# Kernel tuning notes

Measured on AMD Instinct MI355X. Metric: run time of the kernel, lower is better.

## Reference

```python
import jax, jax.numpy as jnp
import numpy as np

N = 262144   # collocation points (512x512 grid equivalent)
H = 64       # MLP hidden width
PI = np.float32(np.pi)


def setup_inputs() -> dict:
    key = jax.random.key(0)
    ks = jax.random.split(key, 6)
    def glorot(k, shp):
        scale = np.float32(np.sqrt(2.0 / (shp[0] + shp[1])))
        return jax.random.normal(k, shp, jnp.float32) * scale
    return {
        "points": jax.random.uniform(ks[0], (N, 2), jnp.float32),  # (x, t) in [0,1]^2
        "W1": glorot(ks[1], (2, H)), "b1": jnp.zeros((H,), jnp.float32),
        "W2": glorot(ks[2], (H, H)), "b2": jnp.zeros((H,), jnp.float32),
        "W3": glorot(ks[3], (H, H)), "b3": jnp.zeros((H,), jnp.float32),
        "Wo": glorot(ks[4], (H, 1)), "bo": jnp.zeros((1,), jnp.float32),
    }


def _mlp(pt, W1, b1, W2, b2, W3, b3, Wo, bo):
    # pt: [2] -> scalar u(x, t)
    h = jnp.tanh(pt @ W1 + b1)
    h = jnp.tanh(h @ W2 + b2)
    h = jnp.tanh(h @ W3 + b3)
    return (h @ Wo + bo)[0]


def reference(points, W1, b1, W2, b2, W3, b3, Wo, bo):
    params = (W1, b1, W2, b2, W3, b3, Wo, bo)
    dt = points.dtype
    keep_t = jnp.array([0.0, 1.0], dt)   # points * [0,1]
    set_x1 = jnp.array([1.0, 0.0], dt)   # + [1,0] -> (1, t)

    def psi_fn(pt):
        x, t = pt[0], pt[1]
        pt1t = pt * keep_t + set_x1                    # boundary point (1, t)
        u = _mlp(pt, *params)                          # u(x, t)
        u_1t = _mlp(pt1t, *params)                     # u(1, t)
        u1t_x = jax.grad(lambda p: _mlp(p, *params))(pt1t)[0]  # du/dx at (1, t)
        return (2.0 * x * jnp.sin(PI * t)
                + (t * t - t) * (x * x - x) * (u - u_1t - u1t_x))

    def loss_point(pt):
        x, t = pt[0], pt[1]
        psi, g1 = jax.value_and_grad(psi_fn)(pt)       # g1 = (psi_x, psi_t)
        # TF's tape.gradient sums over components of dpsi_dxdt, so:
        # h = grad(psi_x + psi_t) = (psi_xx + psi_tx, psi_xt + psi_tt)
        h = jax.grad(lambda p: jnp.sum(jax.grad(psi_fn)(p)))(pt)
        s = jnp.sin(PI * t)
        res = (h[0] + h[1] + psi * g1[0]
               - s * (2.0 - PI * PI * x * x + 2.0 * x ** 3 * s))
        return jnp.abs(res)

    return jnp.mean(jax.vmap(loss_point)(points))
```

## Files before the change

### kernel.cpp

```cpp
#include <hip/hip_runtime.h>
#include <math.h>

typedef _Float16 half_t;
typedef half_t half8 __attribute__((ext_vector_type(8)));
typedef __fp16 fp16x2 __attribute__((ext_vector_type(2)));
typedef float f32x4 __attribute__((ext_vector_type(4)));
typedef float f32x2 __attribute__((ext_vector_type(2)));

#define PI_F 3.14159265358979323846f

__device__ __forceinline__ f32x2 splat2(float s) { return f32x2{s, s}; }
__device__ __forceinline__ f32x2 fma2(f32x2 a, f32x2 b, f32x2 c) {
    return __builtin_elementwise_fma(a, b, c);
}

__device__ __forceinline__ f32x2 ftanh2(f32x2 z) {
    const f32x2 m = z * splat2(2.8853900817779268f);
    f32x2 t;
    t[0] = exp2f(m[0]);
    t[1] = exp2f(m[1]);
    const f32x2 s = t + splat2(1.f);
    f32x2 r;
    r[0] = __builtin_amdgcn_rcpf(s[0]);
    r[1] = __builtin_amdgcn_rcpf(s[1]);
    return fma2(splat2(-2.f), r, splat2(1.f));
}

__global__ __launch_bounds__(256) void pinn_main(
    const float* __restrict__ pts,
    const float* __restrict__ W1, const float* __restrict__ b1,
    const float* __restrict__ b2, const float* __restrict__ b3,
    const half_t* __restrict__ wsH,
    float* __restrict__ partial)
{
    __shared__ __align__(16) half_t J[192 * 64];
    __shared__ float ubuf[9][16];

    const int tid = threadIdx.x;
    const int l   = tid & 63;
    const int w   = tid >> 6;
    const int q   = l >> 4;
    const int i   = l & 15;
    const int ja  = w * 16 + i;
    const int jb  = w * 16 + q * 4;

    const int rb0 = i * 64 + ((q ^ (i & 7)) << 3);
    const int rb1 = i * 64 + (((4 + q) ^ (i & 7)) << 3);
    const int wbase = i * 64 + ((((w * 2 + (q >> 1)) ^ (i & 7))) << 3) + (q & 1) * 4;

    const half8 w2a = *(const half8*)(wsH + ja * 64 + q * 8);
    const half8 w2b = *(const half8*)(wsH + ja * 64 + 32 + q * 8);
    const half8 w3a = *(const half8*)(wsH + 4096 + ja * 64 + q * 8);
    const half8 w3b = *(const half8*)(wsH + 4096 + ja * 64 + 32 + q * 8);

    const float4 w04 = *(const float4*)(W1 + jb);
    const float4 w14 = *(const float4*)(W1 + 64 + jb);
    const float4 b14 = *(const float4*)(b1 + jb);
    const float4 b24 = *(const float4*)(b2 + jb);
    const float4 b34 = *(const float4*)(b3 + jb);

    half8 wo0 = {0, 0, 0, 0, 0, 0, 0, 0};
    half8 wo1 = {0, 0, 0, 0, 0, 0, 0, 0};
    if (i == 0) {
        wo0 = *(const half8*)(wsH + 8192 + q * 8);
        wo1 = *(const half8*)(wsH + 8192 + 32 + q * 8);
    }

    auto stc = [&](int c, f32x2 v01, f32x2 v23) {
        uint2 d;
        d.x = __builtin_bit_cast(unsigned int,
                                 __builtin_amdgcn_cvt_pkrtz(v01[0], v01[1]));
        d.y = __builtin_bit_cast(unsigned int,
                                 __builtin_amdgcn_cvt_pkrtz(v23[0], v23[1]));
        *(uint2*)(&J[wbase + c * 1024]) = d;
    };

    const f32x2 w0a = {w04.x, w04.y}, w0b = {w04.z, w04.w};
    const f32x2 w1a = {w14.x, w14.y}, w1b = {w14.z, w14.w};
    const f32x2 bba = {b14.x, b14.y}, bbb = {b14.z, b14.w};

    float bsum = 0.f;

    #pragma unroll 1
    for (int pass = 0; pass < 2; ++pass) {
        const int pbase = blockIdx.x * 32 + pass * 16;

        const float2 xy = *(const float2*)(pts + 2 * (pbase + i));
        const float X = xy.x, T = xy.y;

        {
            const f32x2 zva = fma2(splat2(X), w0a, fma2(splat2(T), w1a, bba));
            const f32x2 zvb = fma2(splat2(X), w0b, fma2(splat2(T), w1b, bbb));
            const f32x2 aa = ftanh2(zva), ab = ftanh2(zvb);
            const f32x2 d1a = splat2(1.f) - aa * aa, d1b = splat2(1.f) - ab * ab;
            const f32x2 d2a = splat2(-2.f) * aa * d1a, d2b = splat2(-2.f) * ab * d1b;
            stc(0, aa, ab);
            stc(1, d1a * w0a, d1b * w0b);
            stc(2, d1a * w1a, d1b * w1b);
            stc(3, d2a * w0a * w0a, d2b * w0b * w0b);
            stc(4, d2a * w0a * w1a, d2b * w0b * w1b);
            stc(5, d2a * w1a * w1a, d2b * w1b * w1b);
        }
        {
            const f32x2 zva = fma2(splat2(T), w1a, bba + w0a);
            const f32x2 zvb = fma2(splat2(T), w1b, bbb + w0b);
            const f32x2 aa = ftanh2(zva), ab = ftanh2(zvb);
            const f32x2 e1a = splat2(1.f) - aa * aa, e1b = splat2(1.f) - ab * ab;
            const f32x2 e2a = splat2(-2.f) * aa * e1a, e2b = splat2(-2.f) * ab * e1b;
            const f32x2 e3a = splat2(-2.f) * (e1a * e1a + aa * e2a);
            const f32x2 e3b = splat2(-2.f) * (e1b * e1b + ab * e2b);
            stc(6, aa, ab);
            stc(7, e1a * w0a, e1b * w0b);
            stc(8, e1a * w1a, e1b * w1b);
            stc(9, e2a * w0a * w1a, e2b * w0b * w1b);
            stc(10, e2a * w1a * w1a, e2b * w1b * w1b);
            stc(11, e3a * w0a * w1a * w1a, e3b * w0b * w1b * w1b);
        }

        auto layer_step = [&](const half8 A0, const half8 A1, const float4 b4,
                              bool combine) {
            __syncthreads();
            const f32x4 zb = {b4.x, b4.y, b4.z, b4.w};
            const f32x4 z0 = {0.f, 0.f, 0.f, 0.f};
            f32x4 acc[12];
            #pragma unroll
            for (int c = 0; c < 12; ++c) {
                const half8 f0 = *(const half8*)(&J[rb0 + c * 1024]);
                const half8 f1 = *(const half8*)(&J[rb1 + c * 1024]);
                f32x4 z = (c == 0 || c == 6) ? zb : z0;
                z = __builtin_amdgcn_mfma_f32_16x16x32_f16(A0, f0, z, 0, 0, 0);
                z = __builtin_amdgcn_mfma_f32_16x16x32_f16(A1, f1, z, 0, 0, 0);
                acc[c] = z;
            }
            __syncthreads();

            {
                const f32x2 zva = {acc[0][0], acc[0][1]}, zvb = {acc[0][2], acc[0][3]};
                const f32x2 aa = ftanh2(zva), ab = ftanh2(zvb);
                const f32x2 d1a = splat2(1.f) - aa * aa, d1b = splat2(1.f) - ab * ab;
                const f32x2 d2a = splat2(-2.f) * aa * d1a, d2b = splat2(-2.f) * ab * d1b;
                const f32x2 zxa = {acc[1][0], acc[1][1]}, zxb = {acc[1][2], acc[1][3]};
                const f32x2 zta = {acc[2][0], acc[2][1]}, ztb = {acc[2][2], acc[2][3]};
                const f32x2 zxxa = {acc[3][0], acc[3][1]}, zxxb = {acc[3][2], acc[3][3]};
                const f32x2 zxta = {acc[4][0], acc[4][1]}, zxtb = {acc[4][2], acc[4][3]};
                const f32x2 ztta = {acc[5][0], acc[5][1]}, zttb = {acc[5][2], acc[5][3]};
                stc(0, aa, ab);
                stc(1, d1a * zxa, d1b * zxb);
                stc(2, d1a * zta, d1b * ztb);
                stc(3, fma2(d2a * zxa, zxa, d1a * zxxa), fma2(d2b * zxb, zxb, d1b * zxxb));
                stc(4, fma2(d2a * zxa, zta, d1a * zxta), fma2(d2b * zxb, ztb, d1b * zxtb));
                stc(5, fma2(d2a * zta, zta, d1a * ztta), fma2(d2b * ztb, ztb, d1b * zttb));
            }
            {
                const f32x2 zva = {acc[6][0], acc[6][1]}, zvb = {acc[6][2], acc[6][3]};
                const f32x2 aa = ftanh2(zva), ab = ftanh2(zvb);
                const f32x2 e1a = splat2(1.f) - aa * aa, e1b = splat2(1.f) - ab * ab;
                const f32x2 e2a = splat2(-2.f) * aa * e1a, e2b = splat2(-2.f) * ab * e1b;
                const f32x2 e3a = splat2(-2.f) * (e1a * e1a + aa * e2a);
                const f32x2 e3b = splat2(-2.f) * (e1b * e1b + ab * e2b);
                const f32x2 zxa  = {acc[7][0], acc[7][1]},  zxb  = {acc[7][2], acc[7][3]};
                const f32x2 zta  = {acc[8][0], acc[8][1]},  ztb  = {acc[8][2], acc[8][3]};
                const f32x2 zxta = {acc[9][0], acc[9][1]},  zxtb = {acc[9][2], acc[9][3]};
                const f32x2 ztta = {acc[10][0], acc[10][1]}, zttb = {acc[10][2], acc[10][3]};
                const f32x2 zxtta = {acc[11][0], acc[11][1]}, zxttb = {acc[11][2], acc[11][3]};
                if (combine) {
                    stc(6, aa + e1a * zxa, ab + e1b * zxb);
                    stc(7, fma2(e2a * zxa, zta, fma2(e1a, zxta, e1a * zta)),
                           fma2(e2b * zxb, ztb, fma2(e1b, zxtb, e1b * ztb)));
                    stc(8, fma2(e2a * zta, zta,
                                fma2(e1a, ztta,
                                     fma2(e3a * zxa, zta * zta,
                                          fma2(e2a, fma2(splat2(2.f) * zxta, zta,
                                                         zxa * ztta),
                                               e1a * zxtta)))),
                           fma2(e2b * ztb, ztb,
                                fma2(e1b, zttb,
                                     fma2(e3b * zxb, ztb * ztb,
                                          fma2(e2b, fma2(splat2(2.f) * zxtb, ztb,
                                                         zxb * zttb),
                                               e1b * zxttb)))));
                } else {
                    stc(6, aa, ab);
                    stc(7, e1a * zxa, e1b * zxb);
                    stc(8, e1a * zta, e1b * ztb);
                    stc(9, fma2(e2a * zxa, zta, e1a * zxta),
                           fma2(e2b * zxb, ztb, e1b * zxtb));
                    stc(10, fma2(e2a * zta, zta, e1a * ztta),
                            fma2(e2b * ztb, ztb, e1b * zttb));
                    stc(11,
                        fma2(e3a * zxa, zta * zta,
                             fma2(e2a, fma2(splat2(2.f) * zxta, zta, zxa * ztta),
                                  e1a * zxtta)),
                        fma2(e3b * zxb, ztb * ztb,
                             fma2(e2b, fma2(splat2(2.f) * zxtb, ztb, zxb * zttb),
                                  e1b * zxttb)));
                }
            }
        };
        layer_step(w2a, w2b, b24, false);
        layer_step(w3a, w3b, b34, true);
        __syncthreads();

        if (w < 3) {
            #pragma unroll
            for (int k3 = 0; k3 < 3; ++k3) {
                const int c = w * 3 + k3;
                const half8 f0 = *(const half8*)(&J[rb0 + c * 1024]);
                const half8 f1 = *(const half8*)(&J[rb1 + c * 1024]);
                f32x4 z = {0.f, 0.f, 0.f, 0.f};
                z = __builtin_amdgcn_mfma_f32_16x16x32_f16(wo0, f0, z, 0, 0, 0);
                z = __builtin_amdgcn_mfma_f32_16x16x32_f16(wo1, f1, z, 0, 0, 0);
                if (q == 0) ubuf[c][i] = z[0];
            }
        }
        __syncthreads();

        if (tid < 16) {
            const float x = X, t = T;
            float U[9];
            #pragma unroll
            for (int c = 0; c < 9; ++c) U[c] = ubuf[c][tid];

            const float D   = U[0] - U[6];
            const float Dx  = U[1];
            const float Dt  = U[2] - U[7];
            const float Dxx = U[3];
            const float Dxt = U[4];
            const float Dtt = U[5] - U[8];

            const float s  = __builtin_amdgcn_sinf(0.5f * t);
            const float cc = __builtin_amdgcn_cosf(0.5f * t);
            const float A  = t * t - t,  Ap = 2.f * t - 1.f;
            const float B  = x * x - x,  Bp = 2.f * x - 1.f;

            const float psi    = 2.f * x * s + A * B * D;
            const float psi_x  = 2.f * s + A * (Bp * D + B * Dx);
            const float psi_xx = A * (2.f * D + 2.f * Bp * Dx + B * Dxx);
            const float psi_xt = 2.f * PI_F * cc + Ap * (Bp * D + B * Dx)
                               + A * (Bp * Dt + B * Dxt);
            const float psi_tt = -2.f * PI_F * PI_F * x * s + 2.f * B * D
                               + 2.f * Ap * B * Dt + A * B * Dtt;

            const float forcing = s * (2.f - PI_F * PI_F * x * x
                                       + 2.f * x * x * x * s);
            float s4 = fabsf(psi_xx + 2.f * psi_xt + psi_tt + psi * psi_x - forcing);
            s4 += __shfl_xor(s4, 1, 64);
            s4 += __shfl_xor(s4, 2, 64);
            s4 += __shfl_xor(s4, 4, 64);
            s4 += __shfl_xor(s4, 8, 64);
            if (tid == 0) bsum += s4;
        }
    }

    if (tid == 0) partial[blockIdx.x] = bsum;
}

__global__ __launch_bounds__(256) void pinn_prep(
    const float* __restrict__ W2, const float* __restrict__ W3,
    const float* __restrict__ Wo, half_t* __restrict__ wsH)
{
    const int tid = threadIdx.x;
    for (int idx = tid; idx < 4096; idx += 256) {
        const int n = idx >> 6, k = idx & 63;
        wsH[idx]        = (half_t)W2[k * 64 + n];
        wsH[4096 + idx] = (half_t)W3[k * 64 + n];
    }
    if (tid < 64) wsH[8192 + tid] = (half_t)Wo[tid];
}

__global__ __launch_bounds__(256) void pinn_reduce(
    const float* __restrict__ partial, float* __restrict__ out,
    int nblocks, float invN)
{
    __shared__ float sd[256];
    float s = 0.f;
    for (int i = threadIdx.x; i < nblocks; i += 256) s += partial[i];
    sd[threadIdx.x] = s;
    __syncthreads();
    #pragma unroll
    for (int off = 128; off > 0; off >>= 1) {
        if (threadIdx.x < off) sd[threadIdx.x] += sd[threadIdx.x + off];
        __syncthreads();
    }
    if (threadIdx.x == 0) out[0] = sd[0] * invN;
}

extern "C" void kernel_launch(void* const* d_in, const int* in_sizes, int n_in,
                              void* d_out, int out_size, void* d_ws, size_t ws_size,
                              hipStream_t stream)
{
    const float* pts = (const float*)d_in[0];
    const float* W1  = (const float*)d_in[1];
    const float* b1  = (const float*)d_in[2];
    const float* W2  = (const float*)d_in[3];
    const float* b2  = (const float*)d_in[4];
    const float* W3  = (const float*)d_in[5];
    const float* b3  = (const float*)d_in[6];
    const float* Wo  = (const float*)d_in[7];

    const int nPts    = in_sizes[0] / 2;
    const int nBlocks = nPts / 32;

    half_t* wsH     = (half_t*)d_ws;
    float*  partial = (float*)((char*)d_ws + 32768);

    pinn_prep<<<1, 256, 0, stream>>>(W2, W3, Wo, wsH);
    pinn_main<<<nBlocks, 256, 0, stream>>>(pts, W1, b1, b2, b3, wsH, partial);
    pinn_reduce<<<1, 256, 0, stream>>>(partial, (float*)d_out, nBlocks,
                                       1.f / (float)nPts);
}
```

Measured before the change: 129.4 us.

## Propagate directional derivative along (1,1) instead of separate x/t second derivatives

```diff
diff --git a/kernel.cpp b/kernel.cpp
--- a/kernel.cpp
+++ b/kernel.cpp
@@ -33,8 +33,8 @@
     const half_t* __restrict__ wsH,
     float* __restrict__ partial)
 {
-    __shared__ __align__(16) half_t J[192 * 64];
-    __shared__ float ubuf[9][16];
+    __shared__ __align__(16) half_t J[160 * 64];
+    __shared__ float ubuf[7][16];
 
     const int tid = threadIdx.x;
     const int l   = tid & 63;
@@ -89,6 +89,7 @@
         const float X = xy.x, T = xy.y;
 
         {
+            const f32x2 wda = w0a + w1a, wdb = w0b + w1b;
             const f32x2 zva = fma2(splat2(X), w0a, fma2(splat2(T), w1a, bba));
             const f32x2 zvb = fma2(splat2(X), w0b, fma2(splat2(T), w1b, bbb));
             const f32x2 aa = ftanh2(zva), ab = ftanh2(zvb);
@@ -96,10 +97,8 @@
             const f32x2 d2a = splat2(-2.f) * aa * d1a, d2b = splat2(-2.f) * ab * d1b;
             stc(0, aa, ab);
             stc(1, d1a * w0a, d1b * w0b);
-            stc(2, d1a * w1a, d1b * w1b);
-            stc(3, d2a * w0a * w0a, d2b * w0b * w0b);
-            stc(4, d2a * w0a * w1a, d2b * w0b * w1b);
-            stc(5, d2a * w1a * w1a, d2b * w1b * w1b);
+            stc(2, d1a * wda, d1b * wdb);
+            stc(3, d2a * wda * wda, d2b * wdb * wdb);
         }
         {
             const f32x2 zva = fma2(splat2(T), w1a, bba + w0a);
@@ -109,12 +108,12 @@
             const f32x2 e2a = splat2(-2.f) * aa * e1a, e2b = splat2(-2.f) * ab * e1b;
             const f32x2 e3a = splat2(-2.f) * (e1a * e1a + aa * e2a);
             const f32x2 e3b = splat2(-2.f) * (e1b * e1b + ab * e2b);
-            stc(6, aa, ab);
-            stc(7, e1a * w0a, e1b * w0b);
-            stc(8, e1a * w1a, e1b * w1b);
-            stc(9, e2a * w0a * w1a, e2b * w0b * w1b);
-            stc(10, e2a * w1a * w1a, e2b * w1b * w1b);
-            stc(11, e3a * w0a * w1a * w1a, e3b * w0b * w1b * w1b);
+            stc(4, aa, ab);
+            stc(5, e1a * w0a, e1b * w0b);
+            stc(6, e1a * w1a, e1b * w1b);
+            stc(7, e2a * w0a * w1a, e2b * w0b * w1b);
+            stc(8, e2a * w1a * w1a, e2b * w1b * w1b);
+            stc(9, e3a * w0a * w1a * w1a, e3b * w0b * w1b * w1b);
         }
 
         auto layer_step = [&](const half8 A0, const half8 A1, const float4 b4,
@@ -122,12 +121,12 @@
             __syncthreads();
             const f32x4 zb = {b4.x, b4.y, b4.z, b4.w};
             const f32x4 z0 = {0.f, 0.f, 0.f, 0.f};
-            f32x4 acc[12];
+            f32x4 acc[10];
             #pragma unroll
-            for (int c = 0; c < 12; ++c) {
+            for (int c = 0; c < 10; ++c) {
                 const half8 f0 = *(const half8*)(&J[rb0 + c * 1024]);
                 const half8 f1 = *(const half8*)(&J[rb1 + c * 1024]);
-                f32x4 z = (c == 0 || c == 6) ? zb : z0;
+                f32x4 z = (c == 0 || c == 4) ? zb : z0;
                 z = __builtin_amdgcn_mfma_f32_16x16x32_f16(A0, f0, z, 0, 0, 0);
                 z = __builtin_amdgcn_mfma_f32_16x16x32_f16(A1, f1, z, 0, 0, 0);
                 acc[c] = z;
@@ -140,34 +139,31 @@
                 const f32x2 d1a = splat2(1.f) - aa * aa, d1b = splat2(1.f) - ab * ab;
                 const f32x2 d2a = splat2(-2.f) * aa * d1a, d2b = splat2(-2.f) * ab * d1b;
                 const f32x2 zxa = {acc[1][0], acc[1][1]}, zxb = {acc[1][2], acc[1][3]};
-                const f32x2 zta = {acc[2][0], acc[2][1]}, ztb = {acc[2][2], acc[2][3]};
-                const f32x2 zxxa = {acc[3][0], acc[3][1]}, zxxb = {acc[3][2], acc[3][3]};
-                const f32x2 zxta = {acc[4][0], acc[4][1]}, zxtb = {acc[4][2], acc[4][3]};
-                const f32x2 ztta = {acc[5][0], acc[5][1]}, zttb = {acc[5][2], acc[5][3]};
+                const f32x2 zda = {acc[2][0], acc[2][1]}, zdb = {acc[2][2], acc[2][3]};
+                const f32x2 zdda = {acc[3][0], acc[3][1]}, zddb = {acc[3][2], acc[3][3]};
                 stc(0, aa, ab);
                 stc(1, d1a * zxa, d1b * zxb);
-                stc(2, d1a * zta, d1b * ztb);
-                stc(3, fma2(d2a * zxa, zxa, d1a * zxxa), fma2(d2b * zxb, zxb, d1b * zxxb));
-                stc(4, fma2(d2a * zxa, zta, d1a * zxta), fma2(d2b * zxb, ztb, d1b * zxtb));
-                stc(5, fma2(d2a * zta, zta, d1a * ztta), fma2(d2b * ztb, ztb, d1b * zttb));
+                stc(2, d1a * zda, d1b * zdb);
+                stc(3, fma2(d2a * zda, zda, d1a * zdda),
+                       fma2(d2b * zdb, zdb, d1b * zddb));
             }
             {
-                const f32x2 zva = {acc[6][0], acc[6][1]}, zvb = {acc[6][2], acc[6][3]};
+                const f32x2 zva = {acc[4][0], acc[4][1]}, zvb = {acc[4][2], acc[4][3]};
                 const f32x2 aa = ftanh2(zva), ab = ftanh2(zvb);
                 const f32x2 e1a = splat2(1.f) - aa * aa, e1b = splat2(1.f) - ab * ab;
                 const f32x2 e2a = splat2(-2.f) * aa * e1a, e2b = splat2(-2.f) * ab * e1b;
                 const f32x2 e3a = splat2(-2.f) * (e1a * e1a + aa * e2a);
                 const f32x2 e3b = splat2(-2.f) * (e1b * e1b + ab * e2b);
-                const f32x2 zxa  = {acc[7][0], acc[7][1]},  zxb  = {acc[7][2], acc[7][3]};
-                const f32x2 zta  = {acc[8][0], acc[8][1]},  ztb  = {acc[8][2], acc[8][3]};
-                const f32x2 zxta = {acc[9][0], acc[9][1]},  zxtb = {acc[9][2], acc[9][3]};
-                const f32x2 ztta = {acc[10][0], acc[10][1]}, zttb = {acc[10][2], acc[10][3]};
-                const f32x2 zxtta = {acc[11][0], acc[11][1]}, zxttb = {acc[11][2], acc[11][3]};
+                const f32x2 zxa  = {acc[5][0], acc[5][1]},  zxb  = {acc[5][2], acc[5][3]};
+                const f32x2 zta  = {acc[6][0], acc[6][1]},  ztb  = {acc[6][2], acc[6][3]};
+                const f32x2 zxta = {acc[7][0], acc[7][1]},  zxtb = {acc[7][2], acc[7][3]};
+                const f32x2 ztta = {acc[8][0], acc[8][1]},  zttb = {acc[8][2], acc[8][3]};
+                const f32x2 zxtta = {acc[9][0], acc[9][1]}, zxttb = {acc[9][2], acc[9][3]};
                 if (combine) {
-                    stc(6, aa + e1a * zxa, ab + e1b * zxb);
-                    stc(7, fma2(e2a * zxa, zta, fma2(e1a, zxta, e1a * zta)),
+                    stc(4, aa + e1a * zxa, ab + e1b * zxb);
+                    stc(5, fma2(e2a * zxa, zta, fma2(e1a, zxta, e1a * zta)),
                            fma2(e2b * zxb, ztb, fma2(e1b, zxtb, e1b * ztb)));
-                    stc(8, fma2(e2a * zta, zta,
+                    stc(6, fma2(e2a * zta, zta,
                                 fma2(e1a, ztta,
                                      fma2(e3a * zxa, zta * zta,
                                           fma2(e2a, fma2(splat2(2.f) * zxta, zta,
@@ -180,14 +176,14 @@
                                                          zxb * zttb),
                                                e1b * zxttb)))));
                 } else {
-                    stc(6, aa, ab);
-                    stc(7, e1a * zxa, e1b * zxb);
-                    stc(8, e1a * zta, e1b * ztb);
-                    stc(9, fma2(e2a * zxa, zta, e1a * zxta),
+                    stc(4, aa, ab);
+                    stc(5, e1a * zxa, e1b * zxb);
+                    stc(6, e1a * zta, e1b * ztb);
+                    stc(7, fma2(e2a * zxa, zta, e1a * zxta),
                            fma2(e2b * zxb, ztb, e1b * zxtb));
-                    stc(10, fma2(e2a * zta, zta, e1a * ztta),
+                    stc(8, fma2(e2a * zta, zta, e1a * ztta),
                             fma2(e2b * ztb, ztb, e1b * zttb));
-                    stc(11,
+                    stc(9,
                         fma2(e3a * zxa, zta * zta,
                              fma2(e2a, fma2(splat2(2.f) * zxta, zta, zxa * ztta),
                                   e1a * zxtta)),
@@ -201,49 +197,49 @@
         layer_step(w3a, w3b, b34, true);
         __syncthreads();
 
-        if (w < 3) {
+        {
             #pragma unroll
-            for (int k3 = 0; k3 < 3; ++k3) {
-                const int c = w * 3 + k3;
-                const half8 f0 = *(const half8*)(&J[rb0 + c * 1024]);
-                const half8 f1 = *(const half8*)(&J[rb1 + c * 1024]);
-                f32x4 z = {0.f, 0.f, 0.f, 0.f};
-                z = __builtin_amdgcn_mfma_f32_16x16x32_f16(wo0, f0, z, 0, 0, 0);
-                z = __builtin_amdgcn_mfma_f32_16x16x32_f16(wo1, f1, z, 0, 0, 0);
-                if (q == 0) ubuf[c][i] = z[0];
+            for (int k3 = 0; k3 < 2; ++k3) {
+                const int c = w * 2 + k3;
+                if (c < 7) {
+                    const half8 f0 = *(const half8*)(&J[rb0 + c * 1024]);
+                    const half8 f1 = *(const half8*)(&J[rb1 + c * 1024]);
+                    f32x4 z = {0.f, 0.f, 0.f, 0.f};
+                    z = __builtin_amdgcn_mfma_f32_16x16x32_f16(wo0, f0, z, 0, 0, 0);
+                    z = __builtin_amdgcn_mfma_f32_16x16x32_f16(wo1, f1, z, 0, 0, 0);
+                    if (q == 0) ubuf[c][i] = z[0];
+                }
             }
         }
         __syncthreads();
 
         if (tid < 16) {
             const float x = X, t = T;
-            float U[9];
+            float U[7];
             #pragma unroll
-            for (int c = 0; c < 9; ++c) U[c] = ubuf[c][tid];
-
-            const float D   = U[0] - U[6];
+            for (int c = 0; c < 7; ++c) U[c] = ubuf[c][tid];
+
+            const float D   = U[0] - U[4];
             const float Dx  = U[1];
-            const float Dt  = U[2] - U[7];
-            const float Dxx = U[3];
-            const float Dxt = U[4];
-            const float Dtt = U[5] - U[8];
+            const float Dd  = U[2] - U[5];
+            const float Ddd = U[3] - U[6];
 
             const float s  = __builtin_amdgcn_sinf(0.5f * t);
             const float cc = __builtin_amdgcn_cosf(0.5f * t);
             const float A  = t * t - t,  Ap = 2.f * t - 1.f;
             const float B  = x * x - x,  Bp = 2.f * x - 1.f;
 
-            const float psi    = 2.f * x * s + A * B * D;
-            const float psi_x  = 2.f * s + A * (Bp * D + B * Dx);
-            const float psi_xx = A * (2.f * D + 2.f * Bp * Dx + B * Dxx);
-            const float psi_xt = 2.f * PI_F * cc + Ap * (Bp * D + B * Dx)
-                               + A * (Bp * Dt + B * Dxt);
-            const float psi_tt = -2.f * PI_F * PI_F * x * s + 2.f * B * D
-                               + 2.f * Ap * B * Dt + A * B * Dtt;
+            const float psi   = 2.f * x * s + A * B * D;
+            const float psi_x = 2.f * s + A * (Bp * D + B * Dx);
 
             const float forcing = s * (2.f - PI_F * PI_F * x * x
                                        + 2.f * x * x * x * s);
-            float s4 = fabsf(psi_xx + 2.f * psi_xt + psi_tt + psi * psi_x - forcing);
+            const float res = 4.f * PI_F * cc - 2.f * PI_F * PI_F * x * s
+                            + 2.f * (A + B + Ap * Bp) * D
+                            + 2.f * (A * Bp + Ap * B) * Dd
+                            + A * B * Ddd
+                            + psi * psi_x - forcing;
+            float s4 = fabsf(res);
             s4 += __shfl_xor(s4, 1, 64);
             s4 += __shfl_xor(s4, 2, 64);
             s4 += __shfl_xor(s4, 4, 64);
```

Result: faster. 116.9 us, median of 2 (-9.7%).
